# Optimization experiments

Measured on AMD Instinct MI355X. Metric: run time of the kernel, lower is better.

The kernel has to match this reference:

```python
import jax, jax.numpy as jnp
import numpy as np

DIM = 256
D_STATE = 32
EXPAND = 2
E = EXPAND * DIM            # d_inner = 512
DT_RANK = (DIM + 15) // 16  # 16 (mamba default ceil(d_model/16))
D_CONV = 4                  # mamba default causal conv width
B = 4
L = 1024


def layernorm(x, g, b, eps=1e-5):
    m = jnp.mean(x, axis=-1, keepdims=True)
    v = jnp.var(x, axis=-1, keepdims=True)
    return (x - m) / jnp.sqrt(v + eps) * g + b


def dwconv(x_bcl, w, b, pad):
    # x_bcl: [B,C,L], w: [C,1,K] depthwise
    y = jax.lax.conv_general_dilated(
        x_bcl, w, window_strides=(1,), padding=[pad],
        feature_group_count=x_bcl.shape[1],
        dimension_numbers=('NCW', 'OIW', 'NCW'))
    return y + b[None, :, None]


def selective_scan(u, dt, A, Bm, Cm, D):
    # u,dt: [B,L,E]; A: [E,N]; Bm,Cm: [B,L,N]; D: [E]
    dA = jnp.exp(dt[..., None] * A)                                # [B,L,E,N]
    dBu = dt[..., None] * Bm[:, :, None, :] * u[..., None]         # [B,L,E,N]

    def step(h, inp):
        dA_t, dBu_t = inp
        h = dA_t * h + dBu_t
        return h, h

    h0 = jnp.zeros((u.shape[0], E, D_STATE), u.dtype)
    _, hs = jax.lax.scan(step, h0, (dA.transpose(1, 0, 2, 3), dBu.transpose(1, 0, 2, 3)))
    y = jnp.einsum('lben,bln->ble', hs, Cm)                        # [B,L,E]
    return y + u * D


def mamba(x, in_proj_w, ssm_conv_w, ssm_conv_b, x_proj_w,
          dt_proj_w, dt_proj_b, A_log, Dp, out_proj_w):
    xz = x @ in_proj_w.T                     # [B,L,2E]
    xin, z = xz[..., :E], xz[..., E:]
    # causal depthwise conv (pad left D_CONV-1) + SiLU
    xc = dwconv(xin.transpose(0, 2, 1), ssm_conv_w, ssm_conv_b, (D_CONV - 1, 0))
    u = jax.nn.silu(xc).transpose(0, 2, 1)   # [B,L,E]
    dbl = u @ x_proj_w.T                      # [B,L,dt_rank+2N]
    dt_r = dbl[..., :DT_RANK]
    Bm = dbl[..., DT_RANK:DT_RANK + D_STATE]
    Cm = dbl[..., DT_RANK + D_STATE:]
    dt = jax.nn.softplus(dt_r @ dt_proj_w.T + dt_proj_b)  # [B,L,E]
    A = -jnp.exp(A_log)                                    # [E,N]
    y = selective_scan(u, dt, A, Bm, Cm, Dp)
    y = y * jax.nn.silu(z)
    return y @ out_proj_w.T


def setup_inputs() -> dict:
    key = jax.random.key(0)
    ks = jax.random.split(key, 12)
    f = lambda k, s, sc=0.02: jax.random.normal(k, s, jnp.float32) * sc
    dt_init = jnp.exp(jax.random.uniform(ks[10], (E,), jnp.float32,
                                         np.log(1e-3), np.log(1e-1)))
    dt_bias = dt_init + jnp.log(-jnp.expm1(-dt_init))  # inverse softplus
    A_log = jnp.log(jnp.tile(jnp.arange(1, D_STATE + 1, dtype=jnp.float32), (E, 1)))
    return {
        'x': jax.random.normal(ks[0], (B, L, DIM), jnp.float32),
        'norm1_g': jnp.ones((DIM,), jnp.float32), 'norm1_b': jnp.zeros((DIM,), jnp.float32),
        'conv_w': f(ks[1], (DIM, 1, 3), 0.1), 'conv_b': jnp.zeros((DIM,), jnp.float32),
        'in_proj_w': f(ks[2], (2 * E, DIM)),
        'ssm_conv_w': f(ks[3], (E, 1, D_CONV), 0.1), 'ssm_conv_b': jnp.zeros((E,), jnp.float32),
        'x_proj_w': f(ks[4], (DT_RANK + 2 * D_STATE, E)),
        'dt_proj_w': f(ks[5], (E, DT_RANK), 0.1), 'dt_proj_b': dt_bias,
        'A_log': A_log, 'Dp': jnp.ones((E,), jnp.float32),
        'out_proj_w': f(ks[6], (DIM, E)),
        'norm2_g': jnp.ones((DIM,), jnp.float32), 'norm2_b': jnp.zeros((DIM,), jnp.float32),
        'mlp_w1': f(ks[7], (4 * DIM, DIM)), 'mlp_b1': jnp.zeros((4 * DIM,), jnp.float32),
        'mlp_w2': f(ks[8], (DIM, 4 * DIM)), 'mlp_b2': jnp.zeros((DIM,), jnp.float32),
    }


def reference(x, norm1_g, norm1_b, conv_w, conv_b, in_proj_w, ssm_conv_w,
              ssm_conv_b, x_proj_w, dt_proj_w, dt_proj_b, A_log, Dp,
              out_proj_w, norm2_g, norm2_b, mlp_w1, mlp_b1, mlp_w2, mlp_b2):
    res = x
    h = layernorm(x, norm1_g, norm1_b)
    # local depthwise conv, kernel 3, same padding
    h_conv = dwconv(h.transpose(0, 2, 1), conv_w, conv_b, (1, 1)).transpose(0, 2, 1)
    h = mamba(h_conv + h, in_proj_w, ssm_conv_w, ssm_conv_b, x_proj_w,
              dt_proj_w, dt_proj_b, A_log, Dp, out_proj_w)
    h = res + h  # drop_path = identity (eval)
    m = layernorm(h, norm2_g, norm2_b)
    m = jax.nn.gelu(m @ mlp_w1.T + mlp_b1, approximate=False) @ mlp_w2.T + mlp_b2
    return h + m
```

## Files before the change

kernel.cpp:

```cpp
#include <hip/hip_runtime.h>
#include <hip/hip_bf16.h>
#include <math.h>

#define BATCH 4
#define LSEQ  1024
#define DIM   256
#define ESZ   512
#define NST   32
#define RNK   16
#define MROWS 4096
#define NCH   64
#define CHL   16

typedef __attribute__((ext_vector_type(8))) short bf16x8;
typedef __attribute__((ext_vector_type(4))) float f32x4;

__device__ __forceinline__ float silu_f(float v) { return v / (1.f + __expf(-v)); }
__device__ __forceinline__ float softplus_f(float v) {
    return (v > 20.f) ? v : log1pf(__expf(v));
}

__global__ __launch_bounds__(256) void prep_kernel(
    const float* __restrict__ ipw, const float* __restrict__ opw,
    const float* __restrict__ w1,  const float* __restrict__ w2,
    const float* __restrict__ xpw, __hip_bfloat16* __restrict__ dst,
    const float* __restrict__ x, const float* __restrict__ g,
    const float* __restrict__ b, const float* __restrict__ cw,
    const float* __restrict__ cb, __hip_bfloat16* __restrict__ hm)
{
    if (blockIdx.x < 936) {
        int i = blockIdx.x * 256 + threadIdx.x;
        if (i >= 239616) return;
        const float* s; int off;
        if      (i < 65536)  { s = ipw; off = i; }
        else if (i < 98304)  { s = opw; off = i - 65536; }
        else if (i < 163840) { s = w1;  off = i - 98304; }
        else if (i < 229376) { s = w2;  off = i - 163840; }
        else                 { s = xpw; off = i - 229376; }
        float4 v = ((const float4*)s)[off];
        union { __hip_bfloat16 h[4]; short4 s4; } u;
        u.h[0] = __float2bfloat16(v.x);
        u.h[1] = __float2bfloat16(v.y);
        u.h[2] = __float2bfloat16(v.z);
        u.h[3] = __float2bfloat16(v.w);
        ((short4*)dst)[i] = u.s4;
        return;
    }
    const int row = blockIdx.x - 936;
    const int l   = row & (LSEQ - 1);
    const int d   = threadIdx.x;
    const float gc = g[d], bc = b[d];

    float xc = x[row * DIM + d];
    float xl = (l > 0)        ? x[(row - 1) * DIM + d] : 0.f;
    float xr = (l < LSEQ - 1) ? x[(row + 1) * DIM + d] : 0.f;

    float a[6] = { xc, xc * xc, xl, xl * xl, xr, xr * xr };
    #pragma unroll
    for (int o = 32; o > 0; o >>= 1)
        #pragma unroll
        for (int j = 0; j < 6; ++j) a[j] += __shfl_down(a[j], o, 64);
    __shared__ float red[4][6];
    if ((d & 63) == 0)
        #pragma unroll
        for (int j = 0; j < 6; ++j) red[d >> 6][j] = a[j];
    __syncthreads();
    float t[6];
    #pragma unroll
    for (int j = 0; j < 6; ++j)
        t[j] = red[0][j] + red[1][j] + red[2][j] + red[3][j];

    auto ln = [&](float v, float s, float s2) {
        float m  = s * (1.f / DIM);
        float vr = s2 * (1.f / DIM) - m * m;
        return (v - m) * rsqrtf(vr + 1e-5f) * gc + bc;
    };
    float ln_c = ln(xc, t[0], t[1]);
    float acc  = cw[d * 3 + 1] * ln_c + cb[d] + ln_c;
    if (l > 0)        acc += cw[d * 3 + 0] * ln(xl, t[2], t[3]);
    if (l < LSEQ - 1) acc += cw[d * 3 + 2] * ln(xr, t[4], t[5]);
    hm[row * DIM + d] = __float2bfloat16(acc);
}

__global__ __launch_bounds__(256) void ln_kernel(
    const float* __restrict__ x, const float* __restrict__ g,
    const float* __restrict__ b, __hip_bfloat16* __restrict__ y)
{
    const int row = blockIdx.x;
    const int tid = threadIdx.x;
    float v = x[row * DIM + tid];
    float s = v, s2 = v * v;
    #pragma unroll
    for (int o = 32; o > 0; o >>= 1) {
        s  += __shfl_down(s,  o, 64);
        s2 += __shfl_down(s2, o, 64);
    }
    __shared__ float ls[4], ls2[4];
    if ((tid & 63) == 0) { ls[tid >> 6] = s; ls2[tid >> 6] = s2; }
    __syncthreads();
    float ts  = ls[0]  + ls[1]  + ls[2]  + ls[3];
    float ts2 = ls2[0] + ls2[1] + ls2[2] + ls2[3];
    float mean = ts * (1.f / DIM);
    float var  = ts2 * (1.f / DIM) - mean * mean;
    float inv  = rsqrtf(var + 1e-5f);
    y[row * DIM + tid] =
        __float2bfloat16((v - mean) * inv * g[tid] + b[tid]);
}

__global__ __launch_bounds__(256) void conv4_silu_kernel(
    const __hip_bfloat16* __restrict__ xz, const float* __restrict__ w,
    const float* __restrict__ cb, __hip_bfloat16* __restrict__ ub)
{
    const int i  = blockIdx.x * 256 + threadIdx.x;
    const int e  = i & (ESZ - 1);
    const int bl = i >> 9;
    const int l  = bl & (LSEQ - 1);
    float4 w4 = *(const float4*)(w + e * 4);
    float acc = cb[e];
    {
        int ls;
        ls = l - 3; if (ls >= 0) acc += w4.x * __bfloat162float(xz[(long)(bl - 3) * 1024 + e]);
        ls = l - 2; if (ls >= 0) acc += w4.y * __bfloat162float(xz[(long)(bl - 2) * 1024 + e]);
        ls = l - 1; if (ls >= 0) acc += w4.z * __bfloat162float(xz[(long)(bl - 1) * 1024 + e]);
        acc += w4.w * __bfloat162float(xz[(long)bl * 1024 + e]);
    }
    ub[(long)bl * ESZ + e] = __float2bfloat16(silu_f(acc));
}

#define EPI_NONE      0
#define EPI_GELU      2
#define EPI_RES       3
#define EPI_BIAS_RES  4

template <int BM, int BN, int EPI, int OUT_BF16>
__global__ __launch_bounds__(256) void gemm_lds(
    const __hip_bfloat16* __restrict__ A, int lda,
    const __hip_bfloat16* __restrict__ W, int ldw,
    void* __restrict__ Cout, int ldc, int K,
    const float* __restrict__ bias,
    const float* __restrict__ res, int ldres)
{
    constexpr int BK  = 64;
    constexpr int WTN = BN / 4;
    constexpr int BNF = WTN / 16;
    constexpr int AMF = BM / 16;
    constexpr int AIT = (BM * 8) / 256;
    constexpr int WIT = (BN * 8) / 256;

    __shared__ __hip_bfloat16 As[2][BM * BK];
    __shared__ __hip_bfloat16 Ws[2][BN * BK];

    const int tid  = threadIdx.x;
    const int lane = tid & 63;
    const int wave = tid >> 6;
    const int wn   = wave * WTN;
    const int m0   = blockIdx.x * BM;
    const int n0   = blockIdx.y * BN;
    const int q    = lane >> 4;
    const int lr   = lane & 15;
    const int sx   = (lr & 7) << 4;

    const __hip_bfloat16* Ab = A + (long)m0 * lda;
    const __hip_bfloat16* Wb = W + (long)n0 * ldw;

    f32x4 acc[AMF][BNF];
    #pragma unroll
    for (int i = 0; i < AMF; ++i)
        #pragma unroll
        for (int j = 0; j < BNF; ++j)
            acc[i][j] = (f32x4){0.f, 0.f, 0.f, 0.f};

    auto stage = [&](int s, int k0) {
        #pragma unroll
        for (int it = 0; it < AIT; ++it) {
            const int g   = it * 256 + tid;
            const int row = g >> 3;
            const int scc = (g & 7) ^ (row & 7);
            __builtin_amdgcn_global_load_lds(
                (const __attribute__((address_space(1))) void*)
                    (Ab + (long)row * lda + k0 + scc * 8),
                (__attribute__((address_space(3))) void*)
                    (&As[s][(it * 256 + wave * 64) * 8]),
                16, 0, 0);
        }
        #pragma unroll
        for (int it = 0; it < WIT; ++it) {
            const int g   = it * 256 + tid;
            const int row = g >> 3;
            const int scc = (g & 7) ^ (row & 7);
            __builtin_amdgcn_global_load_lds(
                (const __attribute__((address_space(1))) void*)
                    (Wb + (long)row * ldw + k0 + scc * 8),
                (__attribute__((address_space(3))) void*)
                    (&Ws[s][(it * 256 + wave * 64) * 8]),
                16, 0, 0);
        }
    };

    stage(0, 0);
    __syncthreads();

    int cur = 0;
    for (int k0 = 0; k0 < K; k0 += BK) {
        if (k0 + BK < K) stage(cur ^ 1, k0 + BK);
        #pragma unroll
        for (int ks = 0; ks < 2; ++ks) {
            const int co = (ks * 64 + q * 16) ^ sx;
            bf16x8 af[AMF], bfr[BNF];
            #pragma unroll
            for (int i = 0; i < AMF; ++i)
                af[i] = *(const bf16x8*)(
                    (const char*)&As[cur][0] + (i * 16 + lr) * 128 + co);
            #pragma unroll
            for (int j = 0; j < BNF; ++j)
                bfr[j] = *(const bf16x8*)(
                    (const char*)&Ws[cur][0] + (wn + j * 16 + lr) * 128 + co);
            #pragma unroll
            for (int i = 0; i < AMF; ++i)
                #pragma unroll
                for (int j = 0; j < BNF; ++j)
                    acc[i][j] = __builtin_amdgcn_mfma_f32_16x16x32_bf16(
                        af[i], bfr[j], acc[i][j], 0, 0, 0);
        }
        __syncthreads();
        cur ^= 1;
    }

    #pragma unroll
    for (int i = 0; i < AMF; ++i) {
        #pragma unroll
        for (int j = 0; j < BNF; ++j) {
            const int col  = n0 + wn + j * 16 + lr;
            const int rowb = m0 + i * 16 + q * 4;
            #pragma unroll
            for (int r = 0; r < 4; ++r) {
                const int row = rowb + r;
                float v = acc[i][j][r];
                if (EPI == EPI_GELU) {
                    v += bias[col];
                    v = 0.5f * v * (1.f + erff(v * 0.70710678118654752f));
                } else if (EPI == EPI_RES) {
                    v += res[(long)row * ldres + col];
                } else if (EPI == EPI_BIAS_RES) {
                    v += bias[col] + res[(long)row * ldres + col];
                }
                if (OUT_BF16)
                    ((__hip_bfloat16*)Cout)[(long)row * ldc + col] = __float2bfloat16(v);
                else
                    ((float*)Cout)[(long)row * ldc + col] = v;
            }
        }
    }
}

__global__ __launch_bounds__(256) void xproj_mfma(
    const __hip_bfloat16* __restrict__ A,
    const __hip_bfloat16* __restrict__ W,
    float* __restrict__ C)
{
    constexpr int LS = 72;
    __shared__ __hip_bfloat16 As[64 * LS];
    __shared__ __hip_bfloat16 Ws[80 * LS];
    const int tid  = threadIdx.x;
    const int lane = tid & 63;
    const int wave = tid >> 6;
    const int wm   = wave * 16;
    const int m0   = blockIdx.x * 64;
    const int srow = tid >> 3;
    const int scol = (tid & 7) * 8;
    const int q    = lane >> 4;
    const int lr   = lane & 15;

    f32x4 acc[5];
    #pragma unroll
    for (int j = 0; j < 5; ++j) acc[j] = (f32x4){0.f, 0.f, 0.f, 0.f};

    float4 ar[2], wr[3];
    #pragma unroll
    for (int r = 0; r < 2; ++r)
        ar[r] = *(const float4*)(A + (long)(m0 + r * 32 + srow) * 512 + scol);
    #pragma unroll
    for (int r = 0; r < 3; ++r) {
        int row = r * 32 + srow;
        wr[r] = (row < 80) ? *(const float4*)(W + (long)row * 512 + scol)
                           : make_float4(0.f, 0.f, 0.f, 0.f);
    }

    for (int k0 = 0; k0 < 512; k0 += 64) {
        __syncthreads();
        #pragma unroll
        for (int r = 0; r < 2; ++r)
            *(float4*)(&As[(r * 32 + srow) * LS + scol]) = ar[r];
        #pragma unroll
        for (int r = 0; r < 3; ++r) {
            int row = r * 32 + srow;
            if (row < 80) *(float4*)(&Ws[row * LS + scol]) = wr[r];
        }
        __syncthreads();
        if (k0 + 64 < 512) {
            #pragma unroll
            for (int r = 0; r < 2; ++r)
                ar[r] = *(const float4*)(A + (long)(m0 + r * 32 + srow) * 512 + k0 + 64 + scol);
            #pragma unroll
            for (int r = 0; r < 3; ++r) {
                int row = r * 32 + srow;
                if (row < 80)
                    wr[r] = *(const float4*)(W + (long)row * 512 + k0 + 64 + scol);
            }
        }
        #pragma unroll
        for (int ks = 0; ks < 2; ++ks) {
            bf16x8 af = *(const bf16x8*)(&As[(wm + lr) * LS + ks * 32 + q * 8]);
            #pragma unroll
            for (int j = 0; j < 5; ++j) {
                bf16x8 bf = *(const bf16x8*)(&Ws[(j * 16 + lr) * LS + ks * 32 + q * 8]);
                acc[j] = __builtin_amdgcn_mfma_f32_16x16x32_bf16(af, bf, acc[j], 0, 0, 0);
            }
        }
    }
    #pragma unroll
    for (int j = 0; j < 5; ++j)
        #pragma unroll
        for (int r = 0; r < 4; ++r)
            C[(long)(m0 + wm + q * 4 + r) * 80 + j * 16 + lr] = acc[j][r];
}

__global__ __launch_bounds__(256) void scan_s1(
    const __hip_bfloat16* __restrict__ xz, const float* __restrict__ dbl,
    const float* __restrict__ dtw, const float* __restrict__ dtb,
    const float* __restrict__ A_log,
    const float* __restrict__ scw, const float* __restrict__ scb,
    __hip_bfloat16* __restrict__ P, __hip_bfloat16* __restrict__ Q)
{
    const int tid = threadIdx.x;
    const int e  = ((blockIdx.x & 1) << 8) + tid;
    const int bc = blockIdx.x >> 1;
    const int c  = bc & (NCH - 1);
    const int b  = bc >> 6;

    __shared__ float sD[CHL][80];
    for (int g = tid; g < CHL * 20; g += 256) {
        int r = g / 20, cg = (g % 20) * 4;
        *(float4*)&sD[r][cg] =
            *(const float4*)(dbl + ((long)b * LSEQ + c * CHL + r) * 80 + cg);
    }

    float Aen[NST];
    #pragma unroll
    for (int qd = 0; qd < 8; ++qd) {
        float4 a4 = *(const float4*)(A_log + e * NST + qd * 4);
        Aen[qd * 4 + 0] = -__expf(a4.x);
        Aen[qd * 4 + 1] = -__expf(a4.y);
        Aen[qd * 4 + 2] = -__expf(a4.z);
        Aen[qd * 4 + 3] = -__expf(a4.w);
    }
    float cw4[4];
    #pragma unroll
    for (int k = 0; k < 4; ++k) cw4[k] = scw[e * 4 + k];
    const float cbe = scb[e];

    float4 wq[4];
    #pragma unroll
    for (int qd = 0; qd < 4; ++qd)
        wq[qd] = *(const float4*)(dtw + e * RNK + qd * 4);
    const float dtbe = dtb[e];

    const int l0 = c * CHL;
    const long rowbase = ((long)b * LSEQ) * 1024 + e;
    float xw0, xw1, xw2;
    if (c == 0) { xw0 = xw1 = xw2 = 0.f; }
    else {
        xw0 = __bfloat162float(xz[rowbase + (long)(l0 - 3) * 1024]);
        xw1 = __bfloat162float(xz[rowbase + (long)(l0 - 2) * 1024]);
        xw2 = __bfloat162float(xz[rowbase + (long)(l0 - 1) * 1024]);
    }

    float Pv[NST], Qv[NST];
    #pragma unroll
    for (int n = 0; n < NST; ++n) { Pv[n] = 1.f; Qv[n] = 0.f; }
    __syncthreads();

    for (int t = 0; t < CHL; ++t) {
        const int l = l0 + t;
        float xw3 = __bfloat162float(xz[rowbase + (long)l * 1024]);
        float u = silu_f(cbe + cw4[0]*xw0 + cw4[1]*xw1 + cw4[2]*xw2 + cw4[3]*xw3);
        xw0 = xw1; xw1 = xw2; xw2 = xw3;

        float4 d0 = *(const float4*)&sD[t][0];
        float4 d1 = *(const float4*)&sD[t][4];
        float4 d2 = *(const float4*)&sD[t][8];
        float4 d3 = *(const float4*)&sD[t][12];
        float raw = dtbe
            + wq[0].x*d0.x + wq[0].y*d0.y + wq[0].z*d0.z + wq[0].w*d0.w
            + wq[1].x*d1.x + wq[1].y*d1.y + wq[1].z*d1.z + wq[1].w*d1.w
            + wq[2].x*d2.x + wq[2].y*d2.y + wq[2].z*d2.z + wq[2].w*d2.w
            + wq[3].x*d3.x + wq[3].y*d3.y + wq[3].z*d3.z + wq[3].w*d3.w;
        float dt = softplus_f(raw);
        float xx = dt * u;

        #pragma unroll
        for (int qd = 0; qd < 8; ++qd) {
            float4 b4 = *(const float4*)&sD[t][16 + qd * 4];
            #pragma unroll
            for (int j = 0; j < 4; ++j) {
                const int n = qd * 4 + j;
                float bn = (j == 0) ? b4.x : (j == 1) ? b4.y : (j == 2) ? b4.z : b4.w;
                float dA = __expf(dt * Aen[n]);
                Pv[n] *= dA;
                Qv[n] = fmaf(dA, Qv[n], xx * bn);
            }
        }
    }
    const long pb = ((long)(b * NCH + c) * NST) * ESZ + e;
    #pragma unroll
    for (int n = 0; n < NST; ++n) {
        P[pb + (long)n * ESZ] = __float2bfloat16(Pv[n]);
        Q[pb + (long)n * ESZ] = __float2bfloat16(Qv[n]);
    }
}

__global__ __launch_bounds__(256) void scan_s2(
    __hip_bfloat16* __restrict__ P, const __hip_bfloat16* __restrict__ Q)
{
    const int tg = blockIdx.x * 256 + threadIdx.x;
    const int e  = tg & (ESZ - 1);
    const int n  = (tg >> 9) & (NST - 1);
    const int b  = tg >> 14;
    float h = 0.f;
    #pragma unroll 4
    for (int c = 0; c < NCH; ++c) {
        const long idx = ((long)(b * NCH + c) * NST + n) * ESZ + e;
        float Pv = __bfloat162float(P[idx]);
        float Qv = __bfloat162float(Q[idx]);
        P[idx] = __float2bfloat16(h);
        h = fmaf(Pv, h, Qv);
    }
}

__global__ __launch_bounds__(256) void scan_s3(
    const __hip_bfloat16* __restrict__ xz, const float* __restrict__ dbl,
    const float* __restrict__ dtw, const float* __restrict__ dtb,
    const float* __restrict__ A_log,
    const float* __restrict__ scw, const float* __restrict__ scb,
    const float* __restrict__ Dp, const __hip_bfloat16* __restrict__ H,
    __hip_bfloat16* __restrict__ yg)
{
    const int tid = threadIdx.x;
    const int e  = ((blockIdx.x & 1) << 8) + tid;
    const int bc = blockIdx.x >> 1;
    const int c  = bc & (NCH - 1);
    const int b  = bc >> 6;

    __shared__ float sD[CHL][80];
    for (int g = tid; g < CHL * 20; g += 256) {
        int r = g / 20, cg = (g % 20) * 4;
        *(float4*)&sD[r][cg] =
            *(const float4*)(dbl + ((long)b * LSEQ + c * CHL + r) * 80 + cg);
    }

    float Aen[NST];
    #pragma unroll
    for (int qd = 0; qd < 8; ++qd) {
        float4 a4 = *(const float4*)(A_log + e * NST + qd * 4);
        Aen[qd * 4 + 0] = -__expf(a4.x);
        Aen[qd * 4 + 1] = -__expf(a4.y);
        Aen[qd * 4 + 2] = -__expf(a4.z);
        Aen[qd * 4 + 3] = -__expf(a4.w);
    }
    float cw4[4];
    #pragma unroll
    for (int k = 0; k < 4; ++k) cw4[k] = scw[e * 4 + k];
    const float cbe = scb[e];
    const float dpe = Dp[e];

    float4 wq[4];
    #pragma unroll
    for (int qd = 0; qd < 4; ++qd)
        wq[qd] = *(const float4*)(dtw + e * RNK + qd * 4);
    const float dtbe = dtb[e];

    float h[NST];
    const long pb = ((long)(b * NCH + c) * NST) * ESZ + e;
    #pragma unroll
    for (int n = 0; n < NST; ++n)
        h[n] = __bfloat162float(H[pb + (long)n * ESZ]);

    const int l0 = c * CHL;
    const long rowbase = ((long)b * LSEQ) * 1024 + e;
    float xw0, xw1, xw2;
    if (c == 0) { xw0 = xw1 = xw2 = 0.f; }
    else {
        xw0 = __bfloat162float(xz[rowbase + (long)(l0 - 3) * 1024]);
        xw1 = __bfloat162float(xz[rowbase + (long)(l0 - 2) * 1024]);
        xw2 = __bfloat162float(xz[rowbase + (long)(l0 - 1) * 1024]);
    }
    __syncthreads();

    for (int t = 0; t < CHL; ++t) {
        const int l = l0 + t;
        const long bl = (long)b * LSEQ + l;
        float xw3 = __bfloat162float(xz[rowbase + (long)l * 1024]);
        float u = silu_f(cbe + cw4[0]*xw0 + cw4[1]*xw1 + cw4[2]*xw2 + cw4[3]*xw3);
        xw0 = xw1; xw1 = xw2; xw2 = xw3;

        float4 d0 = *(const float4*)&sD[t][0];
        float4 d1 = *(const float4*)&sD[t][4];
        float4 d2 = *(const float4*)&sD[t][8];
        float4 d3 = *(const float4*)&sD[t][12];
        float raw = dtbe
            + wq[0].x*d0.x + wq[0].y*d0.y + wq[0].z*d0.z + wq[0].w*d0.w
            + wq[1].x*d1.x + wq[1].y*d1.y + wq[1].z*d1.z + wq[1].w*d1.w
            + wq[2].x*d2.x + wq[2].y*d2.y + wq[2].z*d2.z + wq[2].w*d2.w
            + wq[3].x*d3.x + wq[3].y*d3.y + wq[3].z*d3.z + wq[3].w*d3.w;
        float dt = softplus_f(raw);
        float xx = dt * u;

        float y = 0.f;
        #pragma unroll
        for (int qd = 0; qd < 8; ++qd) {
            float4 b4 = *(const float4*)&sD[t][16 + qd * 4];
            float4 c4 = *(const float4*)&sD[t][48 + qd * 4];
            #pragma unroll
            for (int j = 0; j < 4; ++j) {
                const int n = qd * 4 + j;
                float bn = (j == 0) ? b4.x : (j == 1) ? b4.y : (j == 2) ? b4.z : b4.w;
                float cn = (j == 0) ? c4.x : (j == 1) ? c4.y : (j == 2) ? c4.z : c4.w;
                float dA = __expf(dt * Aen[n]);
                h[n] = fmaf(dA, h[n], xx * bn);
                y = fmaf(h[n], cn, y);
            }
        }
        y += u * dpe;
        float z = __bfloat162float(xz[rowbase + (long)l * 1024 + ESZ]);
        yg[bl * ESZ + e] = __float2bfloat16(y * silu_f(z));
    }
}

extern "C" void kernel_launch(void* const* d_in, const int* in_sizes, int n_in,
                              void* d_out, int out_size, void* d_ws, size_t ws_size,
                              hipStream_t stream)
{
    const float* x    = (const float*)d_in[0];
    const float* n1g  = (const float*)d_in[1];
    const float* n1b  = (const float*)d_in[2];
    const float* cw   = (const float*)d_in[3];
    const float* cb   = (const float*)d_in[4];
    const float* ipw  = (const float*)d_in[5];
    const float* scw  = (const float*)d_in[6];
    const float* scb  = (const float*)d_in[7];
    const float* xpw  = (const float*)d_in[8];
    const float* dtw  = (const float*)d_in[9];
    const float* dtbi = (const float*)d_in[10];
    const float* alog = (const float*)d_in[11];
    const float* dp   = (const float*)d_in[12];
    const float* opw  = (const float*)d_in[13];
    const float* n2g  = (const float*)d_in[14];
    const float* n2b  = (const float*)d_in[15];
    const float* w1   = (const float*)d_in[16];
    const float* b1   = (const float*)d_in[17];
    const float* w2   = (const float*)d_in[18];
    const float* b2   = (const float*)d_in[19];
    float* out = (float*)d_out;

    float* ws = (float*)d_ws;
    __hip_bfloat16* hmb  = (__hip_bfloat16*)(ws + 0);
    __hip_bfloat16* xzb  = (__hip_bfloat16*)(ws + 524288);
    __hip_bfloat16* ub   = (__hip_bfloat16*)(ws + 2621440);
    float*          dbl  = ws + 3670016;
    __hip_bfloat16* P    = (__hip_bfloat16*)(ws + 5046272);
    __hip_bfloat16* Q    = (__hip_bfloat16*)(ws + 7143424);
    __hip_bfloat16* ygb  = (__hip_bfloat16*)(ws + 9240576);
    float*          hres = ws + 10289152;
    __hip_bfloat16* h1b  = (__hip_bfloat16*)(ws + 11337728);
    __hip_bfloat16* midb = (__hip_bfloat16*)(ws + 11862016);
    __hip_bfloat16* wb   = (__hip_bfloat16*)(ws + 13959168);
    __hip_bfloat16* ipwb = wb;
    __hip_bfloat16* opwb = wb + 262144;
    __hip_bfloat16* w1b  = wb + 393216;
    __hip_bfloat16* w2b  = wb + 655360;
    __hip_bfloat16* xpwb = wb + 917504;

    prep_kernel<<<5032, 256, 0, stream>>>(ipw, opw, w1, w2, xpw, wb,
                                          x, n1g, n1b, cw, cb, hmb);
    gemm_lds<64, 128, EPI_NONE, 1><<<dim3(64, 8), 256, 0, stream>>>(
        hmb, 256, ipwb, 256, xzb, 1024, 256, nullptr, nullptr, 0);
    conv4_silu_kernel<<<8192, 256, 0, stream>>>(xzb, scw, scb, ub);
    xproj_mfma<<<64, 256, 0, stream>>>(ub, xpwb, dbl);
    scan_s1<<<512, 256, 0, stream>>>(xzb, dbl, dtw, dtbi, alog, scw, scb, P, Q);
    scan_s2<<<256, 256, 0, stream>>>(P, Q);
    scan_s3<<<512, 256, 0, stream>>>(xzb, dbl, dtw, dtbi, alog, scw, scb, dp, P, ygb);
    gemm_lds<64, 64, EPI_RES, 0><<<dim3(64, 4), 256, 0, stream>>>(
        ygb, 512, opwb, 512, hres, 256, 512, nullptr, x, 256);
    ln_kernel<<<MROWS, 256, 0, stream>>>(hres, n2g, n2b, h1b);
    gemm_lds<64, 128, EPI_GELU, 1><<<dim3(64, 8), 256, 0, stream>>>(
        h1b, 256, w1b, 256, midb, 1024, 256, b1, nullptr, 0);
    gemm_lds<64, 64, EPI_BIAS_RES, 0><<<dim3(64, 4), 256, 0, stream>>>(
        midb, 1024, w2b, 1024, out, 256, 1024, b2, hres, 256);
}
```

Before: 238.4 us.

## Fuse causal conv into x_proj GEMM and LayerNorm into out_proj GEMM

Folds the depthwise causal conv and SiLU into the x_proj MFMA kernel's A-tile loader, so the u tensor is no longer written to or read back from global memory. Replaces the out_proj GEMM and the separate LayerNorm kernel with one kernel that computes full 256-wide rows per block, adds the residual, and applies LN2 from LDS. The new kernel uses a double-buffered direct global-to-LDS load path with XOR swizzling. Also raises the unroll factor in scan_s2. The trade-offs are redundant conv work across 64 small blocks and fewer, larger out_proj blocks (256 blocks of 16 rows).

After: 234.3 us. About the same (-1.7%).

```diff
diff --git a/kernel.cpp b/kernel.cpp
--- a/kernel.cpp
+++ b/kernel.cpp
@@ -18,6 +18,15 @@
 __device__ __forceinline__ float silu_f(float v) { return v / (1.f + __expf(-v)); }
 __device__ __forceinline__ float softplus_f(float v) {
     return (v > 20.f) ? v : log1pf(__expf(v));
+}
+__device__ __forceinline__ float bs2f(short s) {
+    union { unsigned int u; float f; } v;
+    v.u = ((unsigned int)(unsigned short)s) << 16;
+    return v.f;
+}
+__device__ __forceinline__ short f2bs(float f) {
+    __hip_bfloat16 h = __float2bfloat16(f);
+    return *(short*)&h;
 }
 
 __global__ __launch_bounds__(256) void prep_kernel(
@@ -82,51 +91,6 @@
     hm[row * DIM + d] = __float2bfloat16(acc);
 }
 
-__global__ __launch_bounds__(256) void ln_kernel(
-    const float* __restrict__ x, const float* __restrict__ g,
-    const float* __restrict__ b, __hip_bfloat16* __restrict__ y)
-{
-    const int row = blockIdx.x;
-    const int tid = threadIdx.x;
-    float v = x[row * DIM + tid];
-    float s = v, s2 = v * v;
-    #pragma unroll
-    for (int o = 32; o > 0; o >>= 1) {
-        s  += __shfl_down(s,  o, 64);
-        s2 += __shfl_down(s2, o, 64);
-    }
-    __shared__ float ls[4], ls2[4];
-    if ((tid & 63) == 0) { ls[tid >> 6] = s; ls2[tid >> 6] = s2; }
-    __syncthreads();
-    float ts  = ls[0]  + ls[1]  + ls[2]  + ls[3];
-    float ts2 = ls2[0] + ls2[1] + ls2[2] + ls2[3];
-    float mean = ts * (1.f / DIM);
-    float var  = ts2 * (1.f / DIM) - mean * mean;
-    float inv  = rsqrtf(var + 1e-5f);
-    y[row * DIM + tid] =
-        __float2bfloat16((v - mean) * inv * g[tid] + b[tid]);
-}
-
-__global__ __launch_bounds__(256) void conv4_silu_kernel(
-    const __hip_bfloat16* __restrict__ xz, const float* __restrict__ w,
-    const float* __restrict__ cb, __hip_bfloat16* __restrict__ ub)
-{
-    const int i  = blockIdx.x * 256 + threadIdx.x;
-    const int e  = i & (ESZ - 1);
-    const int bl = i >> 9;
-    const int l  = bl & (LSEQ - 1);
-    float4 w4 = *(const float4*)(w + e * 4);
-    float acc = cb[e];
-    {
-        int ls;
-        ls = l - 3; if (ls >= 0) acc += w4.x * __bfloat162float(xz[(long)(bl - 3) * 1024 + e]);
-        ls = l - 2; if (ls >= 0) acc += w4.y * __bfloat162float(xz[(long)(bl - 2) * 1024 + e]);
-        ls = l - 1; if (ls >= 0) acc += w4.z * __bfloat162float(xz[(long)(bl - 1) * 1024 + e]);
-        acc += w4.w * __bfloat162float(xz[(long)bl * 1024 + e]);
-    }
-    ub[(long)bl * ESZ + e] = __float2bfloat16(silu_f(acc));
-}
-
 #define EPI_NONE      0
 #define EPI_GELU      2
 #define EPI_RES       3
@@ -253,8 +217,134 @@
     }
 }
 
-__global__ __launch_bounds__(256) void xproj_mfma(
+__global__ __launch_bounds__(256) void outproj_ln_kernel(
     const __hip_bfloat16* __restrict__ A,
+    const __hip_bfloat16* __restrict__ W,
+    const float* __restrict__ xres,
+    const float* __restrict__ g, const float* __restrict__ b,
+    float* __restrict__ hres,
+    __hip_bfloat16* __restrict__ h1)
+{
+    constexpr int BM = 16, BN = 256, BK = 64, K = 512;
+    __shared__ __hip_bfloat16 As[2][BM * BK];
+    __shared__ __hip_bfloat16 Ws[2][BN * BK];
+    __shared__ float lnt[BM][BN + 4];
+    __shared__ float lnm[BM], lni[BM];
+
+    const int tid  = threadIdx.x;
+    const int lane = tid & 63;
+    const int wave = tid >> 6;
+    const int wn   = wave * 64;
+    const int m0   = blockIdx.x * BM;
+    const int q    = lane >> 4;
+    const int lr   = lane & 15;
+    const int sx   = (lr & 7) << 4;
+
+    const __hip_bfloat16* Ab = A + (long)m0 * K;
+
+    f32x4 acc[4];
+    #pragma unroll
+    for (int j = 0; j < 4; ++j) acc[j] = (f32x4){0.f, 0.f, 0.f, 0.f};
+
+    auto stage = [&](int s, int k0) {
+        if (wave < 2) {
+            const int gA  = tid;
+            const int row = gA >> 3;
+            const int scc = (gA & 7) ^ (row & 7);
+            __builtin_amdgcn_global_load_lds(
+                (const __attribute__((address_space(1))) void*)
+                    (Ab + (long)row * K + k0 + scc * 8),
+                (__attribute__((address_space(3))) void*)
+                    (&As[s][(wave * 64) * 8]),
+                16, 0, 0);
+        }
+        #pragma unroll
+        for (int it = 0; it < 8; ++it) {
+            const int gW  = it * 256 + tid;
+            const int row = gW >> 3;
+            const int scc = (gW & 7) ^ (row & 7);
+            __builtin_amdgcn_global_load_lds(
+                (const __attribute__((address_space(1))) void*)
+                    (W + (long)row * K + k0 + scc * 8),
+                (__attribute__((address_space(3))) void*)
+                    (&Ws[s][(it * 256 + wave * 64) * 8]),
+                16, 0, 0);
+        }
+    };
+
+    stage(0, 0);
+    __syncthreads();
+
+    int cur = 0;
+    for (int k0 = 0; k0 < K; k0 += BK) {
+        if (k0 + BK < K) stage(cur ^ 1, k0 + BK);
+        #pragma unroll
+        for (int ks = 0; ks < 2; ++ks) {
+            const int co = (ks * 64 + q * 16) ^ sx;
+            bf16x8 af = *(const bf16x8*)((const char*)&As[cur][0] + lr * 128 + co);
+            #pragma unroll
+            for (int j = 0; j < 4; ++j) {
+                bf16x8 bfr = *(const bf16x8*)(
+                    (const char*)&Ws[cur][0] + (wn + j * 16 + lr) * 128 + co);
+                acc[j] = __builtin_amdgcn_mfma_f32_16x16x32_bf16(af, bfr, acc[j], 0, 0, 0);
+            }
+        }
+        __syncthreads();
+        cur ^= 1;
+    }
+
+    #pragma unroll
+    for (int j = 0; j < 4; ++j) {
+        const int col = wn + j * 16 + lr;
+        #pragma unroll
+        for (int r = 0; r < 4; ++r) {
+            const int row = q * 4 + r;
+            float v = acc[j][r] + xres[(long)(m0 + row) * DIM + col];
+            hres[(long)(m0 + row) * DIM + col] = v;
+            lnt[row][col] = v;
+        }
+    }
+    __syncthreads();
+
+    {
+        const int rr = tid >> 4, cc = tid & 15;
+        float s = 0.f, s2 = 0.f;
+        #pragma unroll
+        for (int k = 0; k < 16; ++k) {
+            float v = lnt[rr][cc + k * 16];
+            s += v; s2 += v * v;
+        }
+        #pragma unroll
+        for (int m = 8; m > 0; m >>= 1) {
+            s  += __shfl_xor(s,  m, 64);
+            s2 += __shfl_xor(s2, m, 64);
+        }
+        if (cc == 0) {
+            float mean = s * (1.f / DIM);
+            float var  = s2 * (1.f / DIM) - mean * mean;
+            lnm[rr] = mean;
+            lni[rr] = rsqrtf(var + 1e-5f);
+        }
+    }
+    __syncthreads();
+
+    #pragma unroll
+    for (int j = 0; j < 4; ++j) {
+        const int col = wn + j * 16 + lr;
+        const float gc = g[col], bc = b[col];
+        #pragma unroll
+        for (int r = 0; r < 4; ++r) {
+            const int row = q * 4 + r;
+            float v = lnt[row][col];
+            h1[(long)(m0 + row) * DIM + col] =
+                __float2bfloat16((v - lnm[row]) * lni[row] * gc + bc);
+        }
+    }
+}
+
+__global__ __launch_bounds__(256) void xproj_conv_mfma(
+    const __hip_bfloat16* __restrict__ xz,
+    const float* __restrict__ scw, const float* __restrict__ scb,
     const __hip_bfloat16* __restrict__ W,
     float* __restrict__ C)
 {
@@ -275,10 +365,38 @@
     #pragma unroll
     for (int j = 0; j < 5; ++j) acc[j] = (f32x4){0.f, 0.f, 0.f, 0.f};
 
-    float4 ar[2], wr[3];
-    #pragma unroll
-    for (int r = 0; r < 2; ++r)
-        ar[r] = *(const float4*)(A + (long)(m0 + r * 32 + srow) * 512 + scol);
+    auto mk_u2 = [&](int k0, bf16x8& u0, bf16x8& u1) {
+        const int e0 = k0 + scol;
+        float4 w4[8]; float cbv[8];
+        #pragma unroll
+        for (int j = 0; j < 8; ++j) {
+            w4[j]  = *(const float4*)(scw + (e0 + j) * 4);
+            cbv[j] = scb[e0 + j];
+        }
+        #pragma unroll
+        for (int r = 0; r < 2; ++r) {
+            const int bl = m0 + r * 32 + srow;
+            const int l  = bl & (LSEQ - 1);
+            const __hip_bfloat16* xp = xz + (long)bl * 1024 + e0;
+            bf16x8 x3 = *(const bf16x8*)(xp);
+            bf16x8 x0 = (l >= 3) ? *(const bf16x8*)(xp - 3 * 1024) : (bf16x8){0,0,0,0,0,0,0,0};
+            bf16x8 x1 = (l >= 2) ? *(const bf16x8*)(xp - 2 * 1024) : (bf16x8){0,0,0,0,0,0,0,0};
+            bf16x8 x2 = (l >= 1) ? *(const bf16x8*)(xp - 1 * 1024) : (bf16x8){0,0,0,0,0,0,0,0};
+            bf16x8 o;
+            #pragma unroll
+            for (int j = 0; j < 8; ++j) {
+                float a = cbv[j]
+                    + w4[j].x * bs2f(x0[j]) + w4[j].y * bs2f(x1[j])
+                    + w4[j].z * bs2f(x2[j]) + w4[j].w * bs2f(x3[j]);
+                o[j] = f2bs(silu_f(a));
+            }
+            if (r == 0) u0 = o; else u1 = o;
+        }
+    };
+
+    bf16x8 uc[2];
+    float4 wr[3];
+    mk_u2(0, uc[0], uc[1]);
     #pragma unroll
     for (int r = 0; r < 3; ++r) {
         int row = r * 32 + srow;
@@ -290,7 +408,7 @@
         __syncthreads();
         #pragma unroll
         for (int r = 0; r < 2; ++r)
-            *(float4*)(&As[(r * 32 + srow) * LS + scol]) = ar[r];
+            *(bf16x8*)(&As[(r * 32 + srow) * LS + scol]) = uc[r];
         #pragma unroll
         for (int r = 0; r < 3; ++r) {
             int row = r * 32 + srow;
@@ -298,9 +416,7 @@
         }
         __syncthreads();
         if (k0 + 64 < 512) {
-            #pragma unroll
-            for (int r = 0; r < 2; ++r)
-                ar[r] = *(const float4*)(A + (long)(m0 + r * 32 + srow) * 512 + k0 + 64 + scol);
+            mk_u2(k0 + 64, uc[0], uc[1]);
             #pragma unroll
             for (int r = 0; r < 3; ++r) {
                 int row = r * 32 + srow;
@@ -427,7 +543,7 @@
     const int n  = (tg >> 9) & (NST - 1);
     const int b  = tg >> 14;
     float h = 0.f;
-    #pragma unroll 4
+    #pragma unroll 16
     for (int c = 0; c < NCH; ++c) {
         const long idx = ((long)(b * NCH + c) * NST + n) * ESZ + e;
         float Pv = __bfloat162float(P[idx]);
@@ -565,7 +681,6 @@
     float* ws = (float*)d_ws;
     __hip_bfloat16* hmb  = (__hip_bfloat16*)(ws + 0);
     __hip_bfloat16* xzb  = (__hip_bfloat16*)(ws + 524288);
-    __hip_bfloat16* ub   = (__hip_bfloat16*)(ws + 2621440);
     float*          dbl  = ws + 3670016;
     __hip_bfloat16* P    = (__hip_bfloat16*)(ws + 5046272);
     __hip_bfloat16* Q    = (__hip_bfloat16*)(ws + 7143424);
@@ -584,14 +699,11 @@
                                           x, n1g, n1b, cw, cb, hmb);
     gemm_lds<64, 128, EPI_NONE, 1><<<dim3(64, 8), 256, 0, stream>>>(
         hmb, 256, ipwb, 256, xzb, 1024, 256, nullptr, nullptr, 0);
-    conv4_silu_kernel<<<8192, 256, 0, stream>>>(xzb, scw, scb, ub);
-    xproj_mfma<<<64, 256, 0, stream>>>(ub, xpwb, dbl);
+    xproj_conv_mfma<<<64, 256, 0, stream>>>(xzb, scw, scb, xpwb, dbl);
     scan_s1<<<512, 256, 0, stream>>>(xzb, dbl, dtw, dtbi, alog, scw, scb, P, Q);
     scan_s2<<<256, 256, 0, stream>>>(P, Q);
     scan_s3<<<512, 256, 0, stream>>>(xzb, dbl, dtw, dtbi, alog, scw, scb, dp, P, ygb);
-    gemm_lds<64, 64, EPI_RES, 0><<<dim3(64, 4), 256, 0, stream>>>(
-        ygb, 512, opwb, 512, hres, 256, 512, nullptr, x, 256);
-    ln_kernel<<<MROWS, 256, 0, stream>>>(hres, n2g, n2b, h1b);
+    outproj_ln_kernel<<<256, 256, 0, stream>>>(ygb, opwb, x, n2g, n2b, hres, h1b);
     gemm_lds<64, 128, EPI_GELU, 1><<<dim3(64, 8), 256, 0, stream>>>(
         h1b, 256, w1b, 256, midb, 1024, 256, b1, nullptr, 0);
     gemm_lds<64, 64, EPI_BIAS_RES, 0><<<dim3(64, 4), 256, 0, stream>>>(
```
